# Performance work log

Hardware: AMD Instinct MI355X
Metric: run time of the kernel (lower is better)

The kernel has to match this reference:

```python
import jax, jax.numpy as jnp
import numpy as np

HEAD_DIM = 64

def setup_inputs() -> dict:
    key = jax.random.key(0)
    kq, kk, kv = jax.random.split(key, 3)
    shape = (2, 4096, 8, HEAD_DIM)  # [B, S, H, D]
    q = jax.random.normal(kq, shape, dtype=jnp.float32)
    k = jax.random.normal(kk, shape, dtype=jnp.float32)
    v = jax.random.normal(kv, shape, dtype=jnp.float32)
    return {"q": q, "k": k, "v": v}

def reference(q, k, v):
    # Single-process path of SimpleRingAttention: standard softmax attention.
    # q,k,v: [B, S, H, D]; scores computed per head.
    scale = 1.0 / jnp.sqrt(jnp.asarray(HEAD_DIM, dtype=q.dtype))
    scores = jnp.einsum('bqhd,bkhd->bhqk', q, k) * scale  # [B,H,S,S]
    attn = jax.nn.softmax(scores, axis=-1)
    out = jnp.einsum('bhqk,bkhd->bqhd', attn, v)  # back to [B,S,H,D]
    return out
```

## Files before the change

### kernel.cpp

```cpp
#include <hip/hip_runtime.h>
#include <hip/hip_bf16.h>

#define B_ 2
#define S_ 4096
#define H_ 8
#define D_ 64
#define BQ 128
#define BK 64

#define GLOBAL_AS __attribute__((address_space(1)))
#define LDS_AS    __attribute__((address_space(3)))

typedef short bf16x8 __attribute__((ext_vector_type(8)));
typedef short bf16x4 __attribute__((ext_vector_type(4)));
typedef float f32x4  __attribute__((ext_vector_type(4)));

#define QSCALE 0.18033688011112043f

__device__ __forceinline__ short f2bf(float f) {
    __bf16 h = (__bf16)f;
    return __builtin_bit_cast(short, h);
}

__device__ __forceinline__ bf16x8 pack8(float4 f0, float4 f1) {
    bf16x8 r;
    r[0]=f2bf(f0.x); r[1]=f2bf(f0.y); r[2]=f2bf(f0.z); r[3]=f2bf(f0.w);
    r[4]=f2bf(f1.x); r[5]=f2bf(f1.y); r[6]=f2bf(f1.z); r[7]=f2bf(f1.w);
    return r;
}

__device__ __forceinline__ bf16x8 pack8s(float4 f0, float4 f1, float s) {
    bf16x8 r;
    r[0]=f2bf(f0.x*s); r[1]=f2bf(f0.y*s); r[2]=f2bf(f0.z*s); r[3]=f2bf(f0.w*s);
    r[4]=f2bf(f1.x*s); r[5]=f2bf(f1.y*s); r[6]=f2bf(f1.z*s); r[7]=f2bf(f1.w*s);
    return r;
}

__global__ __launch_bounds__(256) void cast_kv_kernel(
    const float* __restrict__ kin, const float* __restrict__ vin,
    unsigned short* __restrict__ kb, unsigned short* __restrict__ vtb)
{
    __shared__ float Lf[64][72];
    const int role = blockIdx.z & 1;
    const int b    = blockIdx.z >> 1;
    const int h    = blockIdx.y;
    const int s0   = blockIdx.x * 64;
    const int t    = threadIdx.x;

    if (role == 0) {
        int r = t >> 2, fq = t & 3;
        const float4* gp = (const float4*)(kin + (((size_t)(b*S_ + s0 + r)*H_ + h)*D_ + fq*16));
        bf16x8 o0 = pack8(gp[0], gp[1]);
        bf16x8 o1 = pack8(gp[2], gp[3]);
        unsigned short* ob = kb + ((size_t)(b*H_ + h)*S_ + s0 + r)*D_ + fq*16;
        *(bf16x8*)ob       = o0;
        *(bf16x8*)(ob + 8) = o1;
    } else {
        {
            int r  = t >> 2, fq = t & 3;
            const float4* gp = (const float4*)(vin + (((size_t)(b*S_ + s0 + r)*H_ + h)*D_ + fq*16));
            #pragma unroll
            for (int j = 0; j < 4; ++j)
                *(f32x4*)&Lf[r][fq*16 + 4*j] = (f32x4){gp[j].x, gp[j].y, gp[j].z, gp[j].w};
        }
        __syncthreads();
        {
            int d = t >> 2, sq = t & 3;
            bf16x8 o0, o1;
            #pragma unroll
            for (int j = 0; j < 8; ++j) o0[j] = f2bf(Lf[sq*16 + j][d]);
            #pragma unroll
            for (int j = 0; j < 8; ++j) o1[j] = f2bf(Lf[sq*16 + 8 + j][d]);
            unsigned short* ob = vtb + (((size_t)(b*H_ + h)*D_ + d)*S_ + s0 + sq*16);
            *(bf16x8*)(ob)     = o0;
            *(bf16x8*)(ob + 8) = o1;
        }
    }
}

template<bool SPLIT>
__global__ __launch_bounds__(256, 4) void fattn_kernel(
    const float* __restrict__ q, const unsigned short* __restrict__ kb,
    const unsigned short* __restrict__ vtb, float* __restrict__ out,
    float* __restrict__ Op, float* __restrict__ lw)
{
    __shared__ unsigned short Ks [BK][64];
    __shared__ unsigned short Vts[D_][64];
    __shared__ unsigned short Ps [BQ][64];

    const int tid  = threadIdx.x;
    const int wave = tid >> 6;
    const int lane = tid & 63;
    const int m16  = tid & 15;
    const int quad = (tid & 63) >> 4;

    const int lin  = blockIdx.x + 32*blockIdx.y + 256*blockIdx.z;
    const int nl   = (lin & 7)*(SPLIT ? 128 : 64) + (lin >> 3);
    const int xq   = nl & 31;
    const int h    = (nl >> 5) & 7;
    const int bz   = nl >> 8;
    const int b    = SPLIT ? (bz >> 1) : bz;
    const int half = SPLIT ? (bz & 1)  : 0;
    const int kt0  = half * 32;
    const int nkt  = SPLIT ? 32 : 64;
    const int q0   = xq * BQ;
    const int bS   = b * S_;
    const int wq2  = wave * 32;
    const int r7   = m16 & 7;

    int ksoff[2][4];
    #pragma unroll
    for (int kh = 0; kh < 2; ++kh)
        #pragma unroll
        for (int t4 = 0; t4 < 4; ++t4)
            ksoff[kh][t4] = (t4*16 + m16)*64 + (((kh*4 + quad) ^ r7)*8);
    int proff[2][2];
    #pragma unroll
    for (int n = 0; n < 2; ++n)
        #pragma unroll
        for (int kh = 0; kh < 2; ++kh)
            proff[n][kh] = (wq2 + n*16 + m16)*64 + (((kh*4 + quad) ^ r7)*8);
    int pwoff[2][4];
    #pragma unroll
    for (int n = 0; n < 2; ++n)
        #pragma unroll
        for (int mt = 0; mt < 4; ++mt)
            pwoff[n][mt] = (wq2 + n*16 + m16)*64
                         + (((2*mt + (quad>>1)) ^ r7)*8) + (quad&1)*4;

    const int srow = (lane >> 3);
    const int c8g  = (lane & 7) ^ srow;
    const int wqs  = wave * 16;
    const unsigned short* ksg[2];
    const unsigned short* vtg[2];
    #pragma unroll
    for (int it = 0; it < 2; ++it) {
        int rk = wqs + it*8 + srow;
        ksg[it] = kb  + ((size_t)(b*H_ + h)*S_ + rk)*64 + c8g*8;
        vtg[it] = vtb + ((size_t)(b*H_ + h)*D_ + rk)*(size_t)S_ + c8g*8;
    }

    bf16x8 bq[2][2];
    #pragma unroll
    for (int n = 0; n < 2; ++n) {
        const int qrow = q0 + wq2 + n*16 + m16;
        const float* qp = q + ((size_t)(bS + qrow)*H_ + h)*D_;
        #pragma unroll
        for (int kh = 0; kh < 2; ++kh) {
            const float4* q4 = (const float4*)(qp + kh*32 + quad*8);
            bq[n][kh] = pack8s(q4[0], q4[1], QSCALE);
        }
    }

    const short ONE = 0x3F80;
    bf16x8 ones = { ONE,ONE,ONE,ONE,ONE,ONE,ONE,ONE };

    f32x4 oacc[2][4];
    f32x4 lacc[2];
    #pragma unroll
    for (int n = 0; n < 2; ++n) {
        lacc[n] = (f32x4){0.f,0.f,0.f,0.f};
        #pragma unroll
        for (int dt = 0; dt < 4; ++dt) oacc[n][dt] = (f32x4){0.f,0.f,0.f,0.f};
    }

    for (int i = 0; i < nkt; ++i) {
        const int kt = kt0 + i;
        __syncthreads();

        #pragma unroll
        for (int it = 0; it < 2; ++it) {
            __builtin_amdgcn_global_load_lds(
                (const GLOBAL_AS void*)(ksg[it] + (size_t)kt*BK*64),
                (LDS_AS void*)&Ks[wqs + it*8][0], 16, 0, 0);
            __builtin_amdgcn_global_load_lds(
                (const GLOBAL_AS void*)(vtg[it] + (size_t)kt*BK),
                (LDS_AS void*)&Vts[wqs + it*8][0], 16, 0, 0);
        }
        __syncthreads();

        #pragma unroll
        for (int mt = 0; mt < 4; ++mt) {
            f32x4 s0 = (f32x4){0.f,0.f,0.f,0.f};
            f32x4 s1 = (f32x4){0.f,0.f,0.f,0.f};
            #pragma unroll
            for (int kh = 0; kh < 2; ++kh) {
                bf16x8 aK = *(const bf16x8*)&Ks[0][ksoff[kh][mt]];
                s0 = __builtin_amdgcn_mfma_f32_16x16x32_bf16(aK, bq[0][kh], s0, 0,0,0);
                s1 = __builtin_amdgcn_mfma_f32_16x16x32_bf16(aK, bq[1][kh], s1, 0,0,0);
            }
            bf16x4 p0, p1;
            #pragma unroll
            for (int r = 0; r < 4; ++r) {
                p0[r] = f2bf(__builtin_exp2f(s0[r]));
                p1[r] = f2bf(__builtin_exp2f(s1[r]));
            }
            *(bf16x4*)&Ps[0][pwoff[0][mt]] = p0;
            *(bf16x4*)&Ps[0][pwoff[1][mt]] = p1;
        }

        #pragma unroll
        for (int kh = 0; kh < 2; ++kh) {
            bf16x8 bp0 = *(const bf16x8*)&Ps[0][proff[0][kh]];
            bf16x8 bp1 = *(const bf16x8*)&Ps[0][proff[1][kh]];
            lacc[0] = __builtin_amdgcn_mfma_f32_16x16x32_bf16(ones, bp0, lacc[0], 0,0,0);
            lacc[1] = __builtin_amdgcn_mfma_f32_16x16x32_bf16(ones, bp1, lacc[1], 0,0,0);
            #pragma unroll
            for (int dt = 0; dt < 4; ++dt) {
                bf16x8 aV = *(const bf16x8*)&Vts[0][ksoff[kh][dt]];
                oacc[0][dt] = __builtin_amdgcn_mfma_f32_16x16x32_bf16(aV, bp0, oacc[0][dt], 0,0,0);
                oacc[1][dt] = __builtin_amdgcn_mfma_f32_16x16x32_bf16(aV, bp1, oacc[1][dt], 0,0,0);
            }
        }
    }

    #pragma unroll
    for (int n = 0; n < 2; ++n) {
        const int orow = q0 + wq2 + n*16 + m16;
        if constexpr (SPLIT) {
            float* ob = Op + (size_t)half*((size_t)B_*S_*H_*D_)
                           + ((size_t)(bS + orow)*H_ + h)*D_;
            #pragma unroll
            for (int dt = 0; dt < 4; ++dt) {
                float4 o4 = { oacc[n][dt][0], oacc[n][dt][1],
                              oacc[n][dt][2], oacc[n][dt][3] };
                *(float4*)(ob + dt*16 + quad*4) = o4;
            }
            if (quad == 0)
                lw[(size_t)half*((size_t)B_*S_*H_) + (size_t)(bS + orow)*H_ + h] = lacc[n][0];
        } else {
            const float linv = 1.0f / lacc[n][0];
            float* ob = out + ((size_t)(bS + orow)*H_ + h)*D_;
            #pragma unroll
            for (int dt = 0; dt < 4; ++dt) {
                float4 o4 = { oacc[n][dt][0]*linv, oacc[n][dt][1]*linv,
                              oacc[n][dt][2]*linv, oacc[n][dt][3]*linv };
                *(float4*)(ob + dt*16 + quad*4) = o4;
            }
        }
    }
}

__global__ __launch_bounds__(256) void combine_kernel(
    const float* __restrict__ Op, const float* __restrict__ lw,
    float* __restrict__ out)
{
    const size_t NR = (size_t)B_*S_*H_;
    const size_t NO = NR * D_;
    const int t = threadIdx.x;
    size_t r  = (size_t)blockIdx.x * 16 + (t >> 4);
    int   c4  = t & 15;
    const float4* p0 = (const float4*)(Op + r*D_) + c4;
    const float4* p1 = (const float4*)(Op + NO + r*D_) + c4;
    float linv = 1.0f / (lw[r] + lw[NR + r]);
    float4 a = *p0, b = *p1;
    float4 o = { (a.x+b.x)*linv, (a.y+b.y)*linv, (a.z+b.z)*linv, (a.w+b.w)*linv };
    *((float4*)(out + r*D_) + c4) = o;
}

#define FBQ 64
#define LDK 72
__global__ __launch_bounds__(256, 4) void fattn_fb(
    const float* __restrict__ q, const float* __restrict__ k,
    const float* __restrict__ v, float* __restrict__ out)
{
    __shared__ unsigned short Ks [BK][LDK];
    __shared__ unsigned short Vts[D_][LDK];
    __shared__ unsigned short Ps [FBQ][LDK];
    const int tid  = threadIdx.x;
    const int wave = tid >> 6;
    const int m16  = tid & 15;
    const int quad = (tid & 63) >> 4;
    const int h    = blockIdx.y;
    const int b    = blockIdx.z;
    const int q0   = blockIdx.x * FBQ;
    const int bS   = b * S_;
    const int wq   = wave * 16;
    bf16x8 bq[2];
    {
        const int qrow = q0 + wq + m16;
        const float* qb = q + ((size_t)(bS + qrow)*H_ + h)*D_;
        #pragma unroll
        for (int kh = 0; kh < 2; ++kh) {
            const float4* qp = (const float4*)(qb + kh*32 + quad*8);
            bq[kh] = pack8s(qp[0], qp[1], QSCALE);
        }
    }
    const short ONE = 0x3F80;
    bf16x8 ones = { ONE,ONE,ONE,ONE,ONE,ONE,ONE,ONE };
    f32x4 oacc[4];
    f32x4 lacc = (f32x4){0.f,0.f,0.f,0.f};
    #pragma unroll
    for (int dt = 0; dt < 4; ++dt) oacc[dt] = (f32x4){0.f,0.f,0.f,0.f};
    const int vd  = tid & 63;
    const int vkg = tid >> 6;
    for (int kt = 0; kt < S_/BK; ++kt) {
        const int k0 = kt * BK;
        __syncthreads();
        #pragma unroll
        for (int i = 0; i < 2; ++i) {
            int chunk = tid + i*256;
            int row = chunk >> 3, c8 = chunk & 7;
            const float4* gp = (const float4*)(k + ((size_t)(bS + k0 + row)*H_ + h)*D_ + c8*8);
            *(bf16x8*)&Ks[row][c8*8] = pack8(gp[0], gp[1]);
        }
        {
            const float* vb = v + ((size_t)(bS + k0 + vkg*16)*H_ + h)*D_ + vd;
            bf16x8 t0, t1;
            #pragma unroll
            for (int i = 0; i < 8; ++i) t0[i] = f2bf(vb[(size_t)i * (H_*D_)]);
            #pragma unroll
            for (int i = 0; i < 8; ++i) t1[i] = f2bf(vb[(size_t)(i+8) * (H_*D_)]);
            *(bf16x8*)&Vts[vd][vkg*16]     = t0;
            *(bf16x8*)&Vts[vd][vkg*16 + 8] = t1;
        }
        __syncthreads();
        f32x4 sacc[4];
        #pragma unroll
        for (int mt = 0; mt < 4; ++mt) sacc[mt] = (f32x4){0.f,0.f,0.f,0.f};
        #pragma unroll
        for (int kh = 0; kh < 2; ++kh)
            #pragma unroll
            for (int mt = 0; mt < 4; ++mt) {
                bf16x8 aK = *(const bf16x8*)&Ks[mt*16 + m16][kh*32 + quad*8];
                sacc[mt] = __builtin_amdgcn_mfma_f32_16x16x32_bf16(aK, bq[kh], sacc[mt], 0,0,0);
            }
        #pragma unroll
        for (int mt = 0; mt < 4; ++mt) {
            bf16x4 pk;
            #pragma unroll
            for (int r = 0; r < 4; ++r)
                pk[r] = f2bf(__builtin_exp2f(sacc[mt][r]));
            *(bf16x4*)&Ps[wq + m16][mt*16 + quad*4] = pk;
        }
        #pragma unroll
        for (int kh = 0; kh < 2; ++kh) {
            bf16x8 bp = *(const bf16x8*)&Ps[wq + m16][kh*32 + quad*8];
            lacc = __builtin_amdgcn_mfma_f32_16x16x32_bf16(ones, bp, lacc, 0,0,0);
            #pragma unroll
            for (int dt = 0; dt < 4; ++dt) {
                bf16x8 aV = *(const bf16x8*)&Vts[dt*16 + m16][kh*32 + quad*8];
                oacc[dt] = __builtin_amdgcn_mfma_f32_16x16x32_bf16(aV, bp, oacc[dt], 0,0,0);
            }
        }
    }
    const float linv = 1.0f / lacc[0];
    const int orow = q0 + wq + m16;
    float* ob = out + ((size_t)(bS + orow)*H_ + h)*D_;
    #pragma unroll
    for (int dt = 0; dt < 4; ++dt) {
        float4 o4 = { oacc[dt][0]*linv, oacc[dt][1]*linv,
                      oacc[dt][2]*linv, oacc[dt][3]*linv };
        *(float4*)(ob + dt*16 + quad*4) = o4;
    }
}

extern "C" void kernel_launch(void* const* d_in, const int* in_sizes, int n_in,
                              void* d_out, int out_size, void* d_ws, size_t ws_size,
                              hipStream_t stream) {
    const float* q = (const float*)d_in[0];
    const float* k = (const float*)d_in[1];
    const float* v = (const float*)d_in[2];
    float* out = (float*)d_out;
    const size_t elems = (size_t)B_*H_*S_*D_;
    const size_t NR    = (size_t)B_*S_*H_;
    const size_t need_cast  = 2 * elems * sizeof(unsigned short);
    const size_t need_split = need_cast + 2*elems*sizeof(float) + 2*NR*sizeof(float);

    if (ws_size >= need_split) {
        unsigned short* kb  = (unsigned short*)d_ws;
        unsigned short* vtb = kb + elems;
        float* Op = (float*)(vtb + elems);
        float* lw = Op + 2*elems;
        cast_kv_kernel<<<dim3(S_/64, H_, B_*2), dim3(256), 0, stream>>>(k, v, kb, vtb);
        fattn_kernel<true><<<dim3(S_/BQ, H_, B_*2), dim3(256), 0, stream>>>(
            q, kb, vtb, out, Op, lw);
        combine_kernel<<<dim3((int)(NR/16)), dim3(256), 0, stream>>>(Op, lw, out);
    } else if (ws_size >= need_cast) {
        unsigned short* kb  = (unsigned short*)d_ws;
        unsigned short* vtb = kb + elems;
        cast_kv_kernel<<<dim3(S_/64, H_, B_*2), dim3(256), 0, stream>>>(k, v, kb, vtb);
        fattn_kernel<false><<<dim3(S_/BQ, H_, B_), dim3(256), 0, stream>>>(
            q, kb, vtb, out, nullptr, nullptr);
    } else {
        fattn_fb<<<dim3(S_/FBQ, H_, B_), dim3(256), 0, stream>>>(q, k, v, out);
    }
}
```

Measured before the change: 195.4 us.

## Fuse K/V bf16 cast into attention kernel with per-tile ready flags

```diff
diff --git a/kernel.cpp b/kernel.cpp
--- a/kernel.cpp
+++ b/kernel.cpp
@@ -78,15 +78,21 @@
     }
 }
 
-template<bool SPLIT>
+template<bool SPLIT, bool FUSED>
 __global__ __launch_bounds__(256, 4) void fattn_kernel(
     const float* __restrict__ q, const unsigned short* __restrict__ kb,
     const unsigned short* __restrict__ vtb, float* __restrict__ out,
-    float* __restrict__ Op, float* __restrict__ lw)
+    float* __restrict__ Op, float* __restrict__ lw,
+    const float* __restrict__ kin, const float* __restrict__ vin,
+    unsigned short* __restrict__ kbw, unsigned short* __restrict__ vtbw,
+    int* __restrict__ flags)
 {
-    __shared__ unsigned short Ks [BK][64];
-    __shared__ unsigned short Vts[D_][64];
-    __shared__ unsigned short Ps [BQ][64];
+    __shared__ union SM {
+        struct { unsigned short Ks[BK][64];
+                 unsigned short Vts[D_][64];
+                 unsigned short Ps[BQ][64]; } m;
+        float Lf[64][72];
+    } sm;
 
     const int tid  = threadIdx.x;
     const int wave = tid >> 6;
@@ -107,6 +113,42 @@
     const int bS   = b * S_;
     const int wq2  = wave * 32;
     const int r7   = m16 & 7;
+    const int slab64 = (b*H_ + h)*64;
+
+    if constexpr (FUSED) {
+        const int ms0 = (kt0 + xq) * BK;
+        const int r = tid >> 2, fq = tid & 3;
+        {
+            const float4* gp = (const float4*)(kin + (((size_t)(bS + ms0 + r)*H_ + h)*D_ + fq*16));
+            bf16x8 o0 = pack8(gp[0], gp[1]);
+            bf16x8 o1 = pack8(gp[2], gp[3]);
+            unsigned short* ob = kbw + ((size_t)(b*H_ + h)*S_ + ms0 + r)*D_ + fq*16;
+            *(bf16x8*)ob       = o0;
+            *(bf16x8*)(ob + 8) = o1;
+        }
+        {
+            const float4* gv = (const float4*)(vin + (((size_t)(bS + ms0 + r)*H_ + h)*D_ + fq*16));
+            #pragma unroll
+            for (int j = 0; j < 4; ++j)
+                *(f32x4*)&sm.Lf[r][fq*16 + 4*j] = (f32x4){gv[j].x, gv[j].y, gv[j].z, gv[j].w};
+        }
+        __syncthreads();
+        {
+            int d = tid >> 2, sq = tid & 3;
+            bf16x8 o0, o1;
+            #pragma unroll
+            for (int j = 0; j < 8; ++j) o0[j] = f2bf(sm.Lf[sq*16 + j][d]);
+            #pragma unroll
+            for (int j = 0; j < 8; ++j) o1[j] = f2bf(sm.Lf[sq*16 + 8 + j][d]);
+            unsigned short* ob = vtbw + (((size_t)(b*H_ + h)*D_ + d)*S_ + ms0 + sq*16);
+            *(bf16x8*)(ob)     = o0;
+            *(bf16x8*)(ob + 8) = o1;
+        }
+        __syncthreads();
+        if (tid == 0)
+            __hip_atomic_store(&flags[slab64 + kt0 + xq], 1,
+                               __ATOMIC_RELEASE, __HIP_MEMORY_SCOPE_AGENT);
+    }
 
     int ksoff[2][4];
     #pragma unroll
@@ -165,17 +207,29 @@
     }
 
     for (int i = 0; i < nkt; ++i) {
-        const int kt = kt0 + i;
+        const int kt = FUSED ? (kt0 + ((xq + i) & 31)) : (kt0 + i);
+
+        if constexpr (FUSED) {
+            if (i > 0 && tid == 0) {
+                int* fp = &flags[slab64 + kt];
+                int spins = 0;
+                while (__hip_atomic_load(fp, __ATOMIC_ACQUIRE,
+                                         __HIP_MEMORY_SCOPE_AGENT) == 0) {
+                    __builtin_amdgcn_s_sleep(8);
+                    if (++spins > (1 << 16)) break;
+                }
+            }
+        }
         __syncthreads();
 
         #pragma unroll
         for (int it = 0; it < 2; ++it) {
             __builtin_amdgcn_global_load_lds(
                 (const GLOBAL_AS void*)(ksg[it] + (size_t)kt*BK*64),
-                (LDS_AS void*)&Ks[wqs + it*8][0], 16, 0, 0);
+                (LDS_AS void*)&sm.m.Ks[wqs + it*8][0], 16, 0, 0);
             __builtin_amdgcn_global_load_lds(
                 (const GLOBAL_AS void*)(vtg[it] + (size_t)kt*BK),
-                (LDS_AS void*)&Vts[wqs + it*8][0], 16, 0, 0);
+                (LDS_AS void*)&sm.m.Vts[wqs + it*8][0], 16, 0, 0);
         }
         __syncthreads();
 
@@ -185,7 +239,7 @@
             f32x4 s1 = (f32x4){0.f,0.f,0.f,0.f};
             #pragma unroll
             for (int kh = 0; kh < 2; ++kh) {
-                bf16x8 aK = *(const bf16x8*)&Ks[0][ksoff[kh][mt]];
+                bf16x8 aK = *(const bf16x8*)&sm.m.Ks[0][ksoff[kh][mt]];
                 s0 = __builtin_amdgcn_mfma_f32_16x16x32_bf16(aK, bq[0][kh], s0, 0,0,0);
                 s1 = __builtin_amdgcn_mfma_f32_16x16x32_bf16(aK, bq[1][kh], s1, 0,0,0);
             }
@@ -195,19 +249,19 @@
                 p0[r] = f2bf(__builtin_exp2f(s0[r]));
                 p1[r] = f2bf(__builtin_exp2f(s1[r]));
             }
-            *(bf16x4*)&Ps[0][pwoff[0][mt]] = p0;
-            *(bf16x4*)&Ps[0][pwoff[1][mt]] = p1;
+            *(bf16x4*)&sm.m.Ps[0][pwoff[0][mt]] = p0;
+            *(bf16x4*)&sm.m.Ps[0][pwoff[1][mt]] = p1;
         }
 
         #pragma unroll
         for (int kh = 0; kh < 2; ++kh) {
-            bf16x8 bp0 = *(const bf16x8*)&Ps[0][proff[0][kh]];
-            bf16x8 bp1 = *(const bf16x8*)&Ps[0][proff[1][kh]];
+            bf16x8 bp0 = *(const bf16x8*)&sm.m.Ps[0][proff[0][kh]];
+            bf16x8 bp1 = *(const bf16x8*)&sm.m.Ps[0][proff[1][kh]];
             lacc[0] = __builtin_amdgcn_mfma_f32_16x16x32_bf16(ones, bp0, lacc[0], 0,0,0);
             lacc[1] = __builtin_amdgcn_mfma_f32_16x16x32_bf16(ones, bp1, lacc[1], 0,0,0);
             #pragma unroll
             for (int dt = 0; dt < 4; ++dt) {
-                bf16x8 aV = *(const bf16x8*)&Vts[0][ksoff[kh][dt]];
+                bf16x8 aV = *(const bf16x8*)&sm.m.Vts[0][ksoff[kh][dt]];
                 oacc[0][dt] = __builtin_amdgcn_mfma_f32_16x16x32_bf16(aV, bp0, oacc[0][dt], 0,0,0);
                 oacc[1][dt] = __builtin_amdgcn_mfma_f32_16x16x32_bf16(aV, bp1, oacc[1][dt], 0,0,0);
             }
@@ -364,24 +418,27 @@
     float* out = (float*)d_out;
     const size_t elems = (size_t)B_*H_*S_*D_;
     const size_t NR    = (size_t)B_*S_*H_;
+    const size_t FLAGS = (size_t)B_*H_*64;
     const size_t need_cast  = 2 * elems * sizeof(unsigned short);
-    const size_t need_split = need_cast + 2*elems*sizeof(float) + 2*NR*sizeof(float);
+    const size_t need_split = need_cast + 2*elems*sizeof(float)
+                            + 2*NR*sizeof(float) + FLAGS*sizeof(int);
 
     if (ws_size >= need_split) {
         unsigned short* kb  = (unsigned short*)d_ws;
         unsigned short* vtb = kb + elems;
         float* Op = (float*)(vtb + elems);
         float* lw = Op + 2*elems;
-        cast_kv_kernel<<<dim3(S_/64, H_, B_*2), dim3(256), 0, stream>>>(k, v, kb, vtb);
-        fattn_kernel<true><<<dim3(S_/BQ, H_, B_*2), dim3(256), 0, stream>>>(
-            q, kb, vtb, out, Op, lw);
+        int* flags = (int*)(lw + 2*NR);
+        hipMemsetAsync(flags, 0, FLAGS*sizeof(int), stream);
+        fattn_kernel<true, true><<<dim3(S_/BQ, H_, B_*2), dim3(256), 0, stream>>>(
+            q, kb, vtb, out, Op, lw, k, v, kb, vtb, flags);
         combine_kernel<<<dim3((int)(NR/16)), dim3(256), 0, stream>>>(Op, lw, out);
     } else if (ws_size >= need_cast) {
         unsigned short* kb  = (unsigned short*)d_ws;
         unsigned short* vtb = kb + elems;
         cast_kv_kernel<<<dim3(S_/64, H_, B_*2), dim3(256), 0, stream>>>(k, v, kb, vtb);
-        fattn_kernel<false><<<dim3(S_/BQ, H_, B_), dim3(256), 0, stream>>>(
-            q, kb, vtb, out, nullptr, nullptr);
+        fattn_kernel<false, false><<<dim3(S_/BQ, H_, B_), dim3(256), 0, stream>>>(
+            q, kb, vtb, out, nullptr, nullptr, nullptr, nullptr, nullptr, nullptr, nullptr);
     } else {
         fattn_fb<<<dim3(S_/FBQ, H_, B_), dim3(256), 0, stream>>>(q, k, v, out);
     }
```

Result: slower. 400.8 us (+105.1%).

## Fuse split-K combine into attention kernel via last-arriver atomic flag

Applied to the files above, without the earlier changes.

```diff
diff --git a/kernel.cpp b/kernel.cpp
--- a/kernel.cpp
+++ b/kernel.cpp
@@ -82,11 +82,12 @@
 __global__ __launch_bounds__(256, 4) void fattn_kernel(
     const float* __restrict__ q, const unsigned short* __restrict__ kb,
     const unsigned short* __restrict__ vtb, float* __restrict__ out,
-    float* __restrict__ Op, float* __restrict__ lw)
+    float* __restrict__ Op, float* __restrict__ lw, int* __restrict__ flags)
 {
     __shared__ unsigned short Ks [BK][64];
     __shared__ unsigned short Vts[D_][64];
     __shared__ unsigned short Ps [BQ][64];
+    __shared__ int s_old;
 
     const int tid  = threadIdx.x;
     const int wave = tid >> 6;
@@ -214,10 +215,10 @@
         }
     }
 
-    #pragma unroll
-    for (int n = 0; n < 2; ++n) {
-        const int orow = q0 + wq2 + n*16 + m16;
-        if constexpr (SPLIT) {
+    if constexpr (SPLIT) {
+        #pragma unroll
+        for (int n = 0; n < 2; ++n) {
+            const int orow = q0 + wq2 + n*16 + m16;
             float* ob = Op + (size_t)half*((size_t)B_*S_*H_*D_)
                            + ((size_t)(bS + orow)*H_ + h)*D_;
             #pragma unroll
@@ -228,7 +229,40 @@
             }
             if (quad == 0)
                 lw[(size_t)half*((size_t)B_*S_*H_) + (size_t)(bS + orow)*H_ + h] = lacc[n][0];
-        } else {
+        }
+        __syncthreads();
+        if (tid == 0)
+            s_old = __hip_atomic_fetch_add(&flags[(b*H_ + h)*32 + xq], 1,
+                                           __ATOMIC_ACQ_REL,
+                                           __HIP_MEMORY_SCOPE_AGENT);
+        __syncthreads();
+        if (s_old == 1) {
+            const int oh = 1 - half;
+            const float* Opp = Op + (size_t)oh*((size_t)B_*S_*H_*D_);
+            const float* lwp = lw + (size_t)oh*((size_t)B_*S_*H_);
+            #pragma unroll
+            for (int n = 0; n < 2; ++n) {
+                const int orow = q0 + wq2 + n*16 + m16;
+                const size_t rbase = ((size_t)(bS + orow)*H_ + h);
+                const float ltp  = lwp[rbase];
+                const float linv = 1.0f / (lacc[n][0] + ltp);
+                const float* pb = Opp + rbase*D_;
+                float* ob = out + rbase*D_;
+                #pragma unroll
+                for (int dt = 0; dt < 4; ++dt) {
+                    float4 p4 = *(const float4*)(pb + dt*16 + quad*4);
+                    float4 o4 = { (oacc[n][dt][0]+p4.x)*linv,
+                                  (oacc[n][dt][1]+p4.y)*linv,
+                                  (oacc[n][dt][2]+p4.z)*linv,
+                                  (oacc[n][dt][3]+p4.w)*linv };
+                    *(float4*)(ob + dt*16 + quad*4) = o4;
+                }
+            }
+        }
+    } else {
+        #pragma unroll
+        for (int n = 0; n < 2; ++n) {
+            const int orow = q0 + wq2 + n*16 + m16;
             const float linv = 1.0f / lacc[n][0];
             float* ob = out + ((size_t)(bS + orow)*H_ + h)*D_;
             #pragma unroll
@@ -239,23 +273,6 @@
             }
         }
     }
-}
-
-__global__ __launch_bounds__(256) void combine_kernel(
-    const float* __restrict__ Op, const float* __restrict__ lw,
-    float* __restrict__ out)
-{
-    const size_t NR = (size_t)B_*S_*H_;
-    const size_t NO = NR * D_;
-    const int t = threadIdx.x;
-    size_t r  = (size_t)blockIdx.x * 16 + (t >> 4);
-    int   c4  = t & 15;
-    const float4* p0 = (const float4*)(Op + r*D_) + c4;
-    const float4* p1 = (const float4*)(Op + NO + r*D_) + c4;
-    float linv = 1.0f / (lw[r] + lw[NR + r]);
-    float4 a = *p0, b = *p1;
-    float4 o = { (a.x+b.x)*linv, (a.y+b.y)*linv, (a.z+b.z)*linv, (a.w+b.w)*linv };
-    *((float4*)(out + r*D_) + c4) = o;
 }
 
 #define FBQ 64
@@ -364,24 +381,27 @@
     float* out = (float*)d_out;
     const size_t elems = (size_t)B_*H_*S_*D_;
     const size_t NR    = (size_t)B_*S_*H_;
+    const size_t NFLAG = (size_t)B_*H_*32;
     const size_t need_cast  = 2 * elems * sizeof(unsigned short);
-    const size_t need_split = need_cast + 2*elems*sizeof(float) + 2*NR*sizeof(float);
+    const size_t need_split = need_cast + 2*elems*sizeof(float)
+                            + 2*NR*sizeof(float) + NFLAG*sizeof(int);
 
     if (ws_size >= need_split) {
         unsigned short* kb  = (unsigned short*)d_ws;
         unsigned short* vtb = kb + elems;
         float* Op = (float*)(vtb + elems);
         float* lw = Op + 2*elems;
+        int* flags = (int*)(lw + 2*NR);
+        hipMemsetAsync(flags, 0, NFLAG*sizeof(int), stream);
         cast_kv_kernel<<<dim3(S_/64, H_, B_*2), dim3(256), 0, stream>>>(k, v, kb, vtb);
         fattn_kernel<true><<<dim3(S_/BQ, H_, B_*2), dim3(256), 0, stream>>>(
-            q, kb, vtb, out, Op, lw);
-        combine_kernel<<<dim3((int)(NR/16)), dim3(256), 0, stream>>>(Op, lw, out);
+            q, kb, vtb, out, Op, lw, flags);
     } else if (ws_size >= need_cast) {
         unsigned short* kb  = (unsigned short*)d_ws;
         unsigned short* vtb = kb + elems;
         cast_kv_kernel<<<dim3(S_/64, H_, B_*2), dim3(256), 0, stream>>>(k, v, kb, vtb);
         fattn_kernel<false><<<dim3(S_/BQ, H_, B_), dim3(256), 0, stream>>>(
-            q, kb, vtb, out, nullptr, nullptr);
+            q, kb, vtb, out, nullptr, nullptr, nullptr);
     } else {
         fattn_fb<<<dim3(S_/FBQ, H_, B_), dim3(256), 0, stream>>>(q, k, v, out);
     }
```

New measurement: 225.2 us. 1.15x slower.
